# Kernel optimization log

Measured on AMD Instinct MI355X. Metric: run time of the kernel, lower is better.

## Reference

```python
import jax, jax.numpy as jnp
import numpy as np

N = 65536      # num ref nodes
M = 65536      # num query nodes
E = 1572864    # num edges (avg degree 24)
K0 = 27        # num kernels (3x3x3 neighborhood)
D1 = 64        # input channels
D2 = 64        # output channels


def setup_inputs() -> dict:
    key = jax.random.key(0)
    k1, k2, k3, k4, k5, k6 = jax.random.split(key, 6)
    # kernel init mirrors initialize_kernel_weight (uniform in [-bound, bound])
    fan_in = D1 * K0
    gain = float(np.sqrt(2.0 / (1.0 + 5.0)))  # leaky_relu gain with slope sqrt(5)
    std = gain / np.sqrt(fan_in)
    bound = float(np.sqrt(3.0) * std)
    kernel = jax.random.uniform(k1, (K0, D1, D2), minval=-bound, maxval=bound, dtype=jnp.float32)
    ref_feat = jax.random.normal(k2, (N, D1), dtype=jnp.float32)
    e_kernel = jax.random.randint(k3, (E,), 0, K0)
    e_ref = jax.random.randint(k4, (E,), 0, N)
    e_query = jax.random.randint(k5, (E,), 0, M)
    e_weight = jax.random.uniform(k6, (E,), dtype=jnp.float32)
    return {
        "kernel": kernel,
        "ref_feat": ref_feat,
        "e_kernel": e_kernel,
        "e_ref": e_ref,
        "e_query": e_query,
        "num_queries": M,
        "e_weight": e_weight,
    }


def reference(kernel, ref_feat, e_kernel, e_ref, e_query, num_queries, e_weight):
    # Math of MessagePassing.forward:
    #   query_feat[m] = sum_{edges e: e_query[e]==m} w_e * (ref_feat[e_ref[e]] @ kernel[e_kernel[e]])
    # Efficient form: precompute each node's transform under every kernel
    # (N*K0*D1*D2 dense GEMM), then gather per edge and scatter-reduce.
    transformed = jnp.einsum('nd,kdo->nko', ref_feat, kernel)   # [N, K0, D2]
    msgs = transformed[e_ref, e_kernel] * e_weight[:, None]      # [E, D2]
    query_feat = jax.ops.segment_sum(msgs, e_query, num_segments=num_queries)  # [M, D2]
    return query_feat
```

## Files before the change

### kernel.cpp

```cpp
#include <hip/hip_runtime.h>

#define DIN 64
#define DOUT 64
#define MAXK 32

typedef __bf16 bf16x8 __attribute__((ext_vector_type(8)));
typedef float  f32x4  __attribute__((ext_vector_type(4)));
typedef unsigned int u32x4 __attribute__((ext_vector_type(4)));

static __device__ inline unsigned short f2b(float x) {
    return __builtin_bit_cast(unsigned short, (__bf16)x);
}
static __device__ inline float b2f(unsigned short u) {
    return __uint_as_float(((unsigned int)u) << 16);
}


__global__ void conv_w_kernel(const float* __restrict__ W,
                              unsigned short* __restrict__ Wt, int total,
                              int* __restrict__ qcount) {
    int i = blockIdx.x * blockDim.x + threadIdx.x;
    if (i < 256) qcount[i] = 0;
    if (i < total) {
        int j    = i & 7;
        int lane = (i >> 3) & 63;
        int h    = (i >> 9) & 1;
        int t    = (i >> 10) & 3;
        int k    = i >> 12;
        int col  = lane & 15;
        int quad = lane >> 4;
        int d1 = h * 32 + quad * 8 + j;
        int d2 = t * 16 + col;
        Wt[i] = f2b(W[(k * 64 + d1) * 64 + d2]);
    }
}


__global__ __launch_bounds__(256) void phaseA_kernel(
    const float* __restrict__ ref,
    const unsigned short* __restrict__ Wt,
    unsigned short* __restrict__ T,
    int K0, int Nn)
{
    const int lane = threadIdx.x & 63;
    const int wid  = threadIdx.x >> 6;
    const int col  = lane & 15;
    const int quad = lane >> 4;
    const int n0   = blockIdx.x * 64 + wid * 16;
    const int row  = n0 + col;

    __shared__ __align__(16) char ldsbuf[4][16 * 144];
    char* buf = ldsbuf[wid];

    const float* rp = ref + (size_t)row * 64;
    f32x4 r0 = *reinterpret_cast<const f32x4*>(rp + quad * 8);
    f32x4 r1 = *reinterpret_cast<const f32x4*>(rp + quad * 8 + 4);
    f32x4 r2 = *reinterpret_cast<const f32x4*>(rp + 32 + quad * 8);
    f32x4 r3 = *reinterpret_cast<const f32x4*>(rp + 32 + quad * 8 + 4);
    bf16x8 b0, b1;
    #pragma unroll
    for (int i = 0; i < 4; ++i) {
        b0[i]     = (__bf16)r0[i];
        b0[4 + i] = (__bf16)r1[i];
        b1[i]     = (__bf16)r2[i];
        b1[4 + i] = (__bf16)r3[i];
    }

    const int rrow = lane >> 2;
    const int rq   = lane & 3;

    for (int k = 0; k < K0; ++k) {
        const unsigned short* Wk = Wt + (size_t)k * 4096;
        #pragma unroll
        for (int t = 0; t < 4; ++t) {
            const unsigned short* ap = Wk + (size_t)t * 1024 + lane * 8;
            bf16x8 a0 = *reinterpret_cast<const bf16x8*>(ap);
            bf16x8 a1 = *reinterpret_cast<const bf16x8*>(ap + 512);
            f32x4 c = {0.f, 0.f, 0.f, 0.f};
            c = __builtin_amdgcn_mfma_f32_16x16x32_bf16(a0, b0, c, 0, 0, 0);
            c = __builtin_amdgcn_mfma_f32_16x16x32_bf16(a1, b1, c, 0, 0, 0);
            unsigned int lo = (unsigned int)f2b(c[0]) | ((unsigned int)f2b(c[1]) << 16);
            unsigned int hi = (unsigned int)f2b(c[2]) | ((unsigned int)f2b(c[3]) << 16);
            *reinterpret_cast<uint2*>(buf + col * 144 + t * 32 + quad * 8) =
                make_uint2(lo, hi);
        }
        u32x4 v0 = *reinterpret_cast<const u32x4*>(buf + rrow * 144 + rq * 32);
        u32x4 v1 = *reinterpret_cast<const u32x4*>(buf + rrow * 144 + rq * 32 + 16);
        size_t gbase = ((size_t)k * Nn + n0 + rrow) * 64 + rq * 16;
        *reinterpret_cast<u32x4*>(T + gbase)     = v0;
        *reinterpret_cast<u32x4*>(T + gbase + 8) = v1;
    }
}


__global__ void p1_hist_kernel(const int* __restrict__ eq, int E,
                               int* __restrict__ qcount) {
    __shared__ int l[256];
    l[threadIdx.x] = 0;
    __syncthreads();
    int stride = gridDim.x * blockDim.x;
    for (int i = blockIdx.x * blockDim.x + threadIdx.x; i < E; i += stride)
        atomicAdd(&l[((unsigned)eq[i]) >> 8], 1);
    __syncthreads();
    int v = l[threadIdx.x];
    if (v) atomicAdd(&qcount[threadIdx.x], v);
}

__global__ void p1_scan_kernel(const int* __restrict__ qcount,
                               int* __restrict__ gbase, int* __restrict__ gcursor,
                               int* __restrict__ qstart, int NB, int M, int E) {
    __shared__ int sh[256];
    int t = threadIdx.x;
    int v = (t < NB) ? qcount[t] : 0;
    sh[t] = v;
    __syncthreads();
    #pragma unroll
    for (int o = 1; o < 256; o <<= 1) {
        int x = (t >= o) ? sh[t - o] : 0;
        __syncthreads();
        sh[t] += x;
        __syncthreads();
    }
    int ex = sh[t] - v;
    if (t < NB) { gbase[t] = ex; gcursor[t] = ex; }
    if (t == 0) qstart[M] = E;
}

__global__ __launch_bounds__(256) void p1_scatter_kernel(
    const int* __restrict__ eq, const int* __restrict__ er,
    const int* __restrict__ ek, const float* __restrict__ ew,
    int E, int* __restrict__ gcursor, uint2* __restrict__ tmp)
{
    __shared__ int bin[256];
    __shared__ int base[256];
    const int t = threadIdx.x;
    bin[t] = 0;
    __syncthreads();
    const int i0 = blockIdx.x * 4096;
    unsigned key[16];
    unsigned rank[16];
    uint2 pay[16];
    #pragma unroll
    for (int u = 0; u < 16; ++u) {
        int i = i0 + u * 256 + t;
        if (i < E) {
            int q = eq[i];
            unsigned b = ((unsigned)q) >> 8;
            key[u] = b;
            rank[u] = atomicAdd(&bin[b], 1);
            pay[u] = make_uint2((unsigned)er[i] | ((unsigned)ek[i] << 16) |
                                ((unsigned)(q & 255) << 21),
                                __float_as_uint(ew[i]));
        } else {
            key[u] = 0xFFFFFFFFu;
        }
    }
    __syncthreads();
    int c = bin[t];
    if (c) base[t] = atomicAdd(&gcursor[t], c);
    __syncthreads();
    #pragma unroll
    for (int u = 0; u < 16; ++u) {
        if (key[u] != 0xFFFFFFFFu)
            tmp[(size_t)base[key[u]] + rank[u]] = pay[u];
    }
}

__global__ __launch_bounds__(256) void p2_kernel(
    const uint2* __restrict__ tmp, const int* __restrict__ gbase,
    const int* __restrict__ qcount, uint2* __restrict__ rec,
    int* __restrict__ qstart)
{
    __shared__ int fine[256];
    __shared__ int foff[256];
    const int b = blockIdx.x;
    const int t = threadIdx.x;
    const int s = gbase[b];
    const int L = qcount[b];
    fine[t] = 0;
    __syncthreads();
    for (int i = t; i < L; i += 256)
        atomicAdd(&fine[(tmp[s + i].x >> 21) & 255], 1);
    __syncthreads();
    int v = fine[t];
    __syncthreads();
    #pragma unroll
    for (int o = 1; o < 256; o <<= 1) {
        int x = (t >= o) ? fine[t - o] : 0;
        __syncthreads();
        fine[t] += x;
        __syncthreads();
    }
    foff[t] = fine[t] - v;
    qstart[b * 256 + t] = s + foff[t];
    __syncthreads();
    fine[t] = 0;
    __syncthreads();
    for (int i = t; i < L; i += 256) {
        uint2 p = tmp[s + i];
        unsigned fb = (p.x >> 21) & 255;
        int r = atomicAdd(&fine[fb], 1);
        rec[(size_t)s + foff[fb] + r] = p;
    }
}


__global__ __launch_bounds__(256) void phaseB_kernel(
    const unsigned short* __restrict__ T,
    const uint2* __restrict__ rec,
    const int* __restrict__ qstart,
    float* __restrict__ out, int Nn)
{
    const int lane = threadIdx.x & 63;
    const int wid  = threadIdx.x >> 6;
    const int q    = blockIdx.x * 4 + wid;

    int beg = qstart[q];
    int end = qstart[q + 1];
    int cnt = end - beg;
    float acc = 0.f;

    if (cnt <= 64) {
        uint2 rv = make_uint2(0u, 0u);
        if (lane < cnt) rv = rec[beg + lane];
        int j = 0;
        for (; j + 8 <= cnt; j += 8) {
            float partial[8];
            #pragma unroll
            for (int u = 0; u < 8; ++u) {
                unsigned mx = (unsigned)__shfl((int)rv.x, j + u);
                unsigned mw = (unsigned)__shfl((int)rv.y, j + u);
                unsigned short tv =
                    T[((size_t)((mx >> 16) & 31) * Nn + (mx & 0xFFFFu)) * 64 + lane];
                partial[u] = __uint_as_float(mw) * b2f(tv);
            }
            #pragma unroll
            for (int u = 0; u < 8; ++u) acc += partial[u];
        }
        for (; j < cnt; ++j) {
            unsigned mx = (unsigned)__shfl((int)rv.x, j);
            unsigned mw = (unsigned)__shfl((int)rv.y, j);
            acc = fmaf(__uint_as_float(mw),
                       b2f(T[((size_t)((mx >> 16) & 31) * Nn + (mx & 0xFFFFu)) * 64 + lane]),
                       acc);
        }
    } else {
        for (int j = beg; j < end; ++j) {
            uint2 v0 = rec[j];
            unsigned m0 = __builtin_amdgcn_readfirstlane(v0.x);
            float w0 = __uint_as_float(__builtin_amdgcn_readfirstlane(v0.y));
            acc = fmaf(w0,
                       b2f(T[((size_t)((m0 >> 16) & 31) * Nn + (m0 & 0xFFFFu)) * 64 + lane]),
                       acc);
        }
    }
    out[(size_t)q * 64 + lane] = acc;
}


__global__ void hist_kernel(const int* __restrict__ ek, int E, int* __restrict__ counts) {
    __shared__ int l[MAXK];
    if (threadIdx.x < MAXK) l[threadIdx.x] = 0;
    __syncthreads();
    int stride = gridDim.x * blockDim.x;
    for (int i = blockIdx.x * blockDim.x + threadIdx.x; i < E; i += stride)
        atomicAdd(&l[ek[i]], 1);
    __syncthreads();
    if (threadIdx.x < MAXK) {
        int v = l[threadIdx.x];
        if (v) atomicAdd(&counts[threadIdx.x], v);
    }
}

__global__ void scan_kernel(const int* __restrict__ counts, int K,
                            int* __restrict__ start, int* __restrict__ cursor) {
    if (threadIdx.x == 0 && blockIdx.x == 0) {
        int acc = 0;
        for (int k = 0; k < K; ++k) {
            start[k] = acc;
            cursor[k] = acc;
            acc += counts[k];
        }
    }
}

__global__ void scatter_kernel(const int* __restrict__ ek, int E,
                               int* __restrict__ cursor, int* __restrict__ sorted) {
    __shared__ int lcnt[MAXK], lbase[MAXK], lpos[MAXK];
    if (threadIdx.x < MAXK) { lcnt[threadIdx.x] = 0; lpos[threadIdx.x] = 0; }
    __syncthreads();
    int i = blockIdx.x * blockDim.x + threadIdx.x;
    int k = 0;
    bool valid = (i < E);
    if (valid) { k = ek[i]; atomicAdd(&lcnt[k], 1); }
    __syncthreads();
    if (threadIdx.x < MAXK) {
        int v = lcnt[threadIdx.x];
        if (v) lbase[threadIdx.x] = atomicAdd(&cursor[threadIdx.x], v);
    }
    __syncthreads();
    if (valid) {
        int slot = lbase[k] + atomicAdd(&lpos[k], 1);
        sorted[slot] = i;
    }
}

__global__ __launch_bounds__(256) void mp_bucket_kernel(
    const float* __restrict__ W, const float* __restrict__ ref,
    const int* __restrict__ e_ref, const int* __restrict__ e_query,
    const float* __restrict__ e_weight, const int* __restrict__ sorted,
    const int* __restrict__ start, const int* __restrict__ counts,
    float* __restrict__ out)
{
    const int k = blockIdx.y;
    const int lane = threadIdx.x & 63;
    const int wid = threadIdx.x >> 6;

    float wreg[DIN];
    const float* Wk = W + k * DIN * DOUT;
    #pragma unroll
    for (int d = 0; d < DIN; ++d) wreg[d] = Wk[d * DOUT + lane];

    const int s = start[k];
    const int c = counts[k];
    const int nwaves = gridDim.x * 4;

    for (int i = blockIdx.x * 4 + wid; i < c; i += nwaves) {
        int eid = __builtin_amdgcn_readfirstlane(sorted[s + i]);
        int r = e_ref[eid];
        int q = e_query[eid];
        float w = e_weight[eid];
        const float* row = ref + r * DIN;
        float a0 = 0.f, a1 = 0.f, a2 = 0.f, a3 = 0.f;
        #pragma unroll
        for (int d = 0; d < DIN; d += 4) {
            a0 += row[d + 0] * wreg[d + 0];
            a1 += row[d + 1] * wreg[d + 1];
            a2 += row[d + 2] * wreg[d + 2];
            a3 += row[d + 3] * wreg[d + 3];
        }
        atomicAdd(&out[q * DOUT + lane], ((a0 + a1) + (a2 + a3)) * w);
    }
}


extern "C" void kernel_launch(void* const* d_in, const int* in_sizes, int n_in,
                              void* d_out, int out_size, void* d_ws, size_t ws_size,
                              hipStream_t stream) {
    const float* W        = (const float*)d_in[0];
    const float* ref      = (const float*)d_in[1];
    const int*   e_kernel = (const int*)d_in[2];
    const int*   e_ref    = (const int*)d_in[3];
    const int*   e_query  = (const int*)d_in[4];
    const float* e_weight = (const float*)d_in[6];

    const int K0 = in_sizes[0] / (DIN * DOUT);
    const int N  = in_sizes[1] / DIN;
    const int E  = in_sizes[2];
    const int M  = out_size / DOUT;
    const int KD = K0 * 64;
    const int NB = M / 256;

    float* out = (float*)d_out;

    size_t off = 0;
    auto alloc = [&](size_t bytes, size_t align) {
        off = (off + align - 1) / align * align;
        size_t r = off; off += bytes; return r;
    };
    size_t o_tmp     = alloc((size_t)E * 8, 16);
    size_t o_rec     = alloc((size_t)E * 8, 16);
    size_t o_qstart  = alloc((size_t)(M + 1) * 4, 4);
    size_t o_qcount  = alloc(256 * 4, 4);
    size_t o_gbase   = alloc(256 * 4, 4);
    size_t o_gcursor = alloc(256 * 4, 4);
    size_t o_wt      = alloc((size_t)K0 * 4096 * 2, 16);
    size_t o_T       = alloc((size_t)N * KD * 2, 16);
    size_t needA = off;

    bool planA_ok = (ws_size >= needA) && (M % 256 == 0) && (NB >= 1) && (NB <= 256) &&
                    (N % 64 == 0) && (N <= 65536) && (K0 <= 32);

    if (planA_ok) {
        char* ws = (char*)d_ws;
        uint2* tmp           = (uint2*)(ws + o_tmp);
        uint2* rec           = (uint2*)(ws + o_rec);
        int*  qstart         = (int*)(ws + o_qstart);
        int*  qcount         = (int*)(ws + o_qcount);
        int*  gbase          = (int*)(ws + o_gbase);
        int*  gcursor        = (int*)(ws + o_gcursor);
        unsigned short* Wt   = (unsigned short*)(ws + o_wt);
        unsigned short* T    = (unsigned short*)(ws + o_T);

        conv_w_kernel<<<(K0 * 4096 + 255) / 256, 256, 0, stream>>>(W, Wt, K0 * 4096,
                                                                   qcount);
        p1_hist_kernel<<<512, 256, 0, stream>>>(e_query, E, qcount);
        p1_scan_kernel<<<1, 256, 0, stream>>>(qcount, gbase, gcursor, qstart, NB, M, E);
        p1_scatter_kernel<<<(E + 4095) / 4096, 256, 0, stream>>>(e_query, e_ref, e_kernel,
                                                                 e_weight, E, gcursor, tmp);
        p2_kernel<<<NB, 256, 0, stream>>>(tmp, gbase, qcount, rec, qstart);

        phaseA_kernel<<<N / 64, 256, 0, stream>>>(ref, Wt, T, K0, N);

        phaseB_kernel<<<M / 4, 256, 0, stream>>>(T, rec, qstart, out, N);
    } else {
        hipMemsetAsync(out, 0, (size_t)out_size * sizeof(float), stream);
        size_t needB = (size_t)(96 + E) * sizeof(int);
        if (ws_size >= needB) {
            int* ws_i   = (int*)d_ws;
            int* counts = ws_i;
            int* start  = ws_i + 32;
            int* cursor = ws_i + 64;
            int* sorted = ws_i + 96;
            hipMemsetAsync(counts, 0, 96 * sizeof(int), stream);
            hist_kernel<<<512, 256, 0, stream>>>(e_kernel, E, counts);
            scan_kernel<<<1, 64, 0, stream>>>(counts, K0, start, cursor);
            scatter_kernel<<<(E + 255) / 256, 256, 0, stream>>>(e_kernel, E, cursor, sorted);
            dim3 grid(64, K0);
            mp_bucket_kernel<<<grid, 256, 0, stream>>>(W, ref, e_ref, e_query, e_weight,
                                                       sorted, start, counts, out);
        }
    }
}
```

Baseline: 276.8 us.

## Co-schedule dense transform blocks with edge scatter and bucket-sort kernels

Phase A (the dense bf16 GEMM that produces T) is split into two halves. Each half is merged into one launch with an independent sorting stage, the coarse edge scatter or the fine per-bucket sort, using blockIdx ranges to choose the role. The aim is to overlap compute-bound GEMM work with memory- and atomic-bound sorting work and to save two kernel launches. Fused blocks reserve LDS for both roles, which may lower occupancy. Phase B also swaps shuffles for readlane scalar broadcasts and uses 32-bit offset arithmetic to cut per-edge address instructions.

New measurement: 269.6 us. -2.6%, faster.

```diff
diff --git a/kernel.cpp b/kernel.cpp
--- a/kernel.cpp
+++ b/kernel.cpp
@@ -36,21 +36,19 @@
 }
 
 
-__global__ __launch_bounds__(256) void phaseA_kernel(
+static __device__ __forceinline__ void phaseA_body(
     const float* __restrict__ ref,
     const unsigned short* __restrict__ Wt,
     unsigned short* __restrict__ T,
-    int K0, int Nn)
+    int K0, int Nn, int nblk, char* lds)
 {
     const int lane = threadIdx.x & 63;
     const int wid  = threadIdx.x >> 6;
     const int col  = lane & 15;
     const int quad = lane >> 4;
-    const int n0   = blockIdx.x * 64 + wid * 16;
+    const int n0   = nblk * 64 + wid * 16;
     const int row  = n0 + col;
-
-    __shared__ __align__(16) char ldsbuf[4][16 * 144];
-    char* buf = ldsbuf[wid];
+    char* buf = lds + wid * (16 * 144);
 
     const float* rp = ref + (size_t)row * 64;
     f32x4 r0 = *reinterpret_cast<const f32x4*>(rp + quad * 8);
@@ -126,17 +124,16 @@
     if (t == 0) qstart[M] = E;
 }
 
-__global__ __launch_bounds__(256) void p1_scatter_kernel(
+static __device__ __forceinline__ void scatter_body(
     const int* __restrict__ eq, const int* __restrict__ er,
     const int* __restrict__ ek, const float* __restrict__ ew,
-    int E, int* __restrict__ gcursor, uint2* __restrict__ tmp)
-{
-    __shared__ int bin[256];
-    __shared__ int base[256];
+    int E, int* __restrict__ gcursor, uint2* __restrict__ tmp,
+    int sblk, int* bin, int* base)
+{
     const int t = threadIdx.x;
     bin[t] = 0;
     __syncthreads();
-    const int i0 = blockIdx.x * 4096;
+    const int i0 = sblk * 4096;
     unsigned key[16];
     unsigned rank[16];
     uint2 pay[16];
@@ -166,14 +163,11 @@
     }
 }
 
-__global__ __launch_bounds__(256) void p2_kernel(
+static __device__ __forceinline__ void p2_body(
     const uint2* __restrict__ tmp, const int* __restrict__ gbase,
     const int* __restrict__ qcount, uint2* __restrict__ rec,
-    int* __restrict__ qstart)
-{
-    __shared__ int fine[256];
-    __shared__ int foff[256];
-    const int b = blockIdx.x;
+    int* __restrict__ qstart, int b, int* fine, int* foff)
+{
     const int t = threadIdx.x;
     const int s = gbase[b];
     const int L = qcount[b];
@@ -201,6 +195,43 @@
         unsigned fb = (p.x >> 21) & 255;
         int r = atomicAdd(&fine[fb], 1);
         rec[(size_t)s + foff[fb] + r] = p;
+    }
+}
+
+
+__global__ __launch_bounds__(256) void fusedA_scatter_kernel(
+    const float* __restrict__ ref, const unsigned short* __restrict__ Wt,
+    unsigned short* __restrict__ T, int K0, int Nn, int NA1,
+    const int* __restrict__ eq, const int* __restrict__ er,
+    const int* __restrict__ ek, const float* __restrict__ ew,
+    int E, int* __restrict__ gcursor, uint2* __restrict__ tmp)
+{
+    __shared__ __align__(16) char ldsbuf[4 * 16 * 144];
+    __shared__ int s0[256];
+    __shared__ int s1[256];
+    if ((int)blockIdx.x < NA1) {
+        phaseA_body(ref, Wt, T, K0, Nn, (int)blockIdx.x, ldsbuf);
+    } else {
+        scatter_body(eq, er, ek, ew, E, gcursor, tmp,
+                     (int)blockIdx.x - NA1, s0, s1);
+    }
+}
+
+__global__ __launch_bounds__(256) void fusedA_p2_kernel(
+    const float* __restrict__ ref, const unsigned short* __restrict__ Wt,
+    unsigned short* __restrict__ T, int K0, int Nn, int NA1, int NA2,
+    const uint2* __restrict__ tmp, const int* __restrict__ gbase,
+    const int* __restrict__ qcount, uint2* __restrict__ rec,
+    int* __restrict__ qstart)
+{
+    __shared__ __align__(16) char ldsbuf[4 * 16 * 144];
+    __shared__ int s0[256];
+    __shared__ int s1[256];
+    if ((int)blockIdx.x < NA2) {
+        phaseA_body(ref, Wt, T, K0, Nn, NA1 + (int)blockIdx.x, ldsbuf);
+    } else {
+        p2_body(tmp, gbase, qcount, rec, qstart,
+                (int)blockIdx.x - NA2, s0, s1);
     }
 }
 
@@ -228,30 +259,30 @@
             float partial[8];
             #pragma unroll
             for (int u = 0; u < 8; ++u) {
-                unsigned mx = (unsigned)__shfl((int)rv.x, j + u);
-                unsigned mw = (unsigned)__shfl((int)rv.y, j + u);
-                unsigned short tv =
-                    T[((size_t)((mx >> 16) & 31) * Nn + (mx & 0xFFFFu)) * 64 + lane];
-                partial[u] = __uint_as_float(mw) * b2f(tv);
+                unsigned mx = (unsigned)__builtin_amdgcn_readlane((int)rv.x, j + u);
+                unsigned mw = (unsigned)__builtin_amdgcn_readlane((int)rv.y, j + u);
+                unsigned off = (((mx >> 16) & 31) * (unsigned)Nn + (mx & 0xFFFFu)) * 64u
+                               + (unsigned)lane;
+                partial[u] = __uint_as_float(mw) * b2f(T[off]);
             }
             #pragma unroll
             for (int u = 0; u < 8; ++u) acc += partial[u];
         }
         for (; j < cnt; ++j) {
-            unsigned mx = (unsigned)__shfl((int)rv.x, j);
-            unsigned mw = (unsigned)__shfl((int)rv.y, j);
-            acc = fmaf(__uint_as_float(mw),
-                       b2f(T[((size_t)((mx >> 16) & 31) * Nn + (mx & 0xFFFFu)) * 64 + lane]),
-                       acc);
+            unsigned mx = (unsigned)__builtin_amdgcn_readlane((int)rv.x, j);
+            unsigned mw = (unsigned)__builtin_amdgcn_readlane((int)rv.y, j);
+            unsigned off = (((mx >> 16) & 31) * (unsigned)Nn + (mx & 0xFFFFu)) * 64u
+                           + (unsigned)lane;
+            acc = fmaf(__uint_as_float(mw), b2f(T[off]), acc);
         }
     } else {
         for (int j = beg; j < end; ++j) {
             uint2 v0 = rec[j];
             unsigned m0 = __builtin_amdgcn_readfirstlane(v0.x);
             float w0 = __uint_as_float(__builtin_amdgcn_readfirstlane(v0.y));
-            acc = fmaf(w0,
-                       b2f(T[((size_t)((m0 >> 16) & 31) * Nn + (m0 & 0xFFFFu)) * 64 + lane]),
-                       acc);
+            unsigned off = (((m0 >> 16) & 31) * (unsigned)Nn + (m0 & 0xFFFFu)) * 64u
+                           + (unsigned)lane;
+            acc = fmaf(w0, b2f(T[off]), acc);
         }
     }
     out[(size_t)q * 64 + lane] = acc;
@@ -392,15 +423,23 @@
         unsigned short* Wt   = (unsigned short*)(ws + o_wt);
         unsigned short* T    = (unsigned short*)(ws + o_T);
 
+        const int NA  = N / 64;
+        const int NA1 = (NA + 1) / 2;
+        const int NA2 = NA - NA1;
+        const int SCB = (E + 4095) / 4096;
+
         conv_w_kernel<<<(K0 * 4096 + 255) / 256, 256, 0, stream>>>(W, Wt, K0 * 4096,
                                                                    qcount);
         p1_hist_kernel<<<512, 256, 0, stream>>>(e_query, E, qcount);
         p1_scan_kernel<<<1, 256, 0, stream>>>(qcount, gbase, gcursor, qstart, NB, M, E);
-        p1_scatter_kernel<<<(E + 4095) / 4096, 256, 0, stream>>>(e_query, e_ref, e_kernel,
-                                                                 e_weight, E, gcursor, tmp);
-        p2_kernel<<<NB, 256, 0, stream>>>(tmp, gbase, qcount, rec, qstart);
-
-        phaseA_kernel<<<N / 64, 256, 0, stream>>>(ref, Wt, T, K0, N);
+
+        fusedA_scatter_kernel<<<NA1 + SCB, 256, 0, stream>>>(
+            ref, Wt, T, K0, N, NA1,
+            e_query, e_ref, e_kernel, e_weight, E, gcursor, tmp);
+
+        fusedA_p2_kernel<<<NA2 + NB, 256, 0, stream>>>(
+            ref, Wt, T, K0, N, NA1, NA2,
+            tmp, gbase, qcount, rec, qstart);
 
         phaseB_kernel<<<M / 4, 256, 0, stream>>>(T, rec, qstart, out, N);
     } else {
```

## Split phase A over kernel chunks, double-buffer LDS staging, use readlane in gather

Applied to the files above, without the earlier changes.

Phase A now runs a 2D grid in which each block handles a quarter of the 27 kernel offsets. This gives four times as many blocks for parallelism, at the cost of each block reloading its ref rows. The per-wave LDS staging buffer is double-buffered by kernel index, so consecutive iterations can overlap their writes and reads. In phase B, __shfl is replaced with scalar readlane broadcasts and 64-bit index math with 32-bit unsigned offsets, which removes LDS-permute and address-arithmetic overhead in the gather loop.

New measurement: 283.3 us. +2.4%, slower.

```diff
diff --git a/kernel.cpp b/kernel.cpp
--- a/kernel.cpp
+++ b/kernel.cpp
@@ -36,7 +36,9 @@
 }
 
 
-__global__ __launch_bounds__(256) void phaseA_kernel(
+#define KSPLIT 4
+
+__global__ __launch_bounds__(256) void phaseA_v3_kernel(
     const float* __restrict__ ref,
     const unsigned short* __restrict__ Wt,
     unsigned short* __restrict__ T,
@@ -49,8 +51,13 @@
     const int n0   = blockIdx.x * 64 + wid * 16;
     const int row  = n0 + col;
 
-    __shared__ __align__(16) char ldsbuf[4][16 * 144];
-    char* buf = ldsbuf[wid];
+    const int kch = (K0 + KSPLIT - 1) / KSPLIT;
+    const int k0  = blockIdx.y * kch;
+    int k1 = k0 + kch;
+    if (k1 > K0) k1 = K0;
+
+    __shared__ __align__(16) char ldsbuf[4 * 2 * 2304];
+    char* bufs = ldsbuf + wid * 2 * 2304;
 
     const float* rp = ref + (size_t)row * 64;
     f32x4 r0 = *reinterpret_cast<const f32x4*>(rp + quad * 8);
@@ -69,7 +76,8 @@
     const int rrow = lane >> 2;
     const int rq   = lane & 3;
 
-    for (int k = 0; k < K0; ++k) {
+    for (int k = k0; k < k1; ++k) {
+        char* buf = bufs + (k & 1) * 2304;
         const unsigned short* Wk = Wt + (size_t)k * 4096;
         #pragma unroll
         for (int t = 0; t < 4; ++t) {
@@ -228,30 +236,30 @@
             float partial[8];
             #pragma unroll
             for (int u = 0; u < 8; ++u) {
-                unsigned mx = (unsigned)__shfl((int)rv.x, j + u);
-                unsigned mw = (unsigned)__shfl((int)rv.y, j + u);
-                unsigned short tv =
-                    T[((size_t)((mx >> 16) & 31) * Nn + (mx & 0xFFFFu)) * 64 + lane];
-                partial[u] = __uint_as_float(mw) * b2f(tv);
+                unsigned mx = (unsigned)__builtin_amdgcn_readlane((int)rv.x, j + u);
+                unsigned mw = (unsigned)__builtin_amdgcn_readlane((int)rv.y, j + u);
+                unsigned off = (((mx >> 16) & 31) * (unsigned)Nn + (mx & 0xFFFFu)) * 64u
+                               + (unsigned)lane;
+                partial[u] = __uint_as_float(mw) * b2f(T[off]);
             }
             #pragma unroll
             for (int u = 0; u < 8; ++u) acc += partial[u];
         }
         for (; j < cnt; ++j) {
-            unsigned mx = (unsigned)__shfl((int)rv.x, j);
-            unsigned mw = (unsigned)__shfl((int)rv.y, j);
-            acc = fmaf(__uint_as_float(mw),
-                       b2f(T[((size_t)((mx >> 16) & 31) * Nn + (mx & 0xFFFFu)) * 64 + lane]),
-                       acc);
+            unsigned mx = (unsigned)__builtin_amdgcn_readlane((int)rv.x, j);
+            unsigned mw = (unsigned)__builtin_amdgcn_readlane((int)rv.y, j);
+            unsigned off = (((mx >> 16) & 31) * (unsigned)Nn + (mx & 0xFFFFu)) * 64u
+                           + (unsigned)lane;
+            acc = fmaf(__uint_as_float(mw), b2f(T[off]), acc);
         }
     } else {
         for (int j = beg; j < end; ++j) {
             uint2 v0 = rec[j];
             unsigned m0 = __builtin_amdgcn_readfirstlane(v0.x);
             float w0 = __uint_as_float(__builtin_amdgcn_readfirstlane(v0.y));
-            acc = fmaf(w0,
-                       b2f(T[((size_t)((m0 >> 16) & 31) * Nn + (m0 & 0xFFFFu)) * 64 + lane]),
-                       acc);
+            unsigned off = (((m0 >> 16) & 31) * (unsigned)Nn + (m0 & 0xFFFFu)) * 64u
+                           + (unsigned)lane;
+            acc = fmaf(w0, b2f(T[off]), acc);
         }
     }
     out[(size_t)q * 64 + lane] = acc;
@@ -400,7 +408,8 @@
                                                                  e_weight, E, gcursor, tmp);
         p2_kernel<<<NB, 256, 0, stream>>>(tmp, gbase, qcount, rec, qstart);
 
-        phaseA_kernel<<<N / 64, 256, 0, stream>>>(ref, Wt, T, K0, N);
+        dim3 agrid(N / 64, KSPLIT);
+        phaseA_v3_kernel<<<agrid, 256, 0, stream>>>(ref, Wt, T, K0, N);
 
         phaseB_kernel<<<M / 4, 256, 0, stream>>>(T, rec, qstart, out, N);
     } else {
```
